# Kernel optimization log

Measured on AMD Instinct MI355X. Metric: run time of the kernel, lower is better.

Reference implementation:

```python
import jax, jax.numpy as jnp
import numpy as np

B, D, N_NEG, N_DOMAINS = 4096, 512, 100, 8
TAU = 1e-4
EPS = 1e-6
REG_W = 1e-4
ALPHA = 0.9


def setup_inputs() -> dict:
    key = jax.random.key(0)
    ks = jax.random.split(key, 12)
    e1 = jax.random.normal(ks[0], (B, D), dtype=jnp.float32)
    e2 = jax.random.normal(ks[1], (B, D), dtype=jnp.float32)
    y_pred = jax.random.normal(ks[2], (B, 1), dtype=jnp.float32)
    y_target = jax.random.normal(ks[3], (B, 1), dtype=jnp.float32)
    # e2_model: Linear(D, D); extra head params only contribute to the L2 reg term
    W_e2 = jax.random.normal(ks[4], (D, D), dtype=jnp.float32) * 0.02
    b_e2 = jax.random.normal(ks[5], (D,), dtype=jnp.float32) * 0.02
    W_head = jax.random.normal(ks[6], (D, 1), dtype=jnp.float32) * 0.02
    b_head = jax.random.normal(ks[7], (1,), dtype=jnp.float32) * 0.02
    # mixup coefficient lambda = (1-alpha)*U[0,1) + alpha, per sample
    lmbda = ALPHA + (1.0 - ALPHA) * jax.random.uniform(ks[8], (B,), dtype=jnp.float32)
    # mixup partner: random index != j (matches vec_neg exclusion in create_aug)
    off = jax.random.randint(ks[9], (B,), 1, B, dtype=jnp.int32)
    mix_idx = (jnp.arange(B, dtype=jnp.int32) + off) % B
    # n random negatives per sample for L_aug
    neg_idx = jax.random.randint(ks[10], (B, N_NEG), 0, B, dtype=jnp.int32)
    domain_tag = jax.random.randint(ks[11], (B,), 0, N_DOMAINS, dtype=jnp.int32)
    return {"e1": e1, "e2": e2, "y_pred": y_pred, "y_target": y_target,
            "W_e2": W_e2, "b_e2": b_e2, "W_head": W_head, "b_head": b_head,
            "lmbda": lmbda, "mix_idx": mix_idx, "neg_idx": neg_idx,
            "domain_tag": domain_tag}


def reference(e1, e2, y_pred, y_target, W_e2, b_e2, W_head, b_head,
              lmbda, mix_idx, neg_idx, domain_tag):
    # --- mse + L2 regularization over all model params ---
    mse_loss = jnp.mean((y_pred - y_target) ** 2)
    reg_loss = REG_W * (jnp.linalg.norm(W_e2) + jnp.linalg.norm(b_e2)
                        + jnp.linalg.norm(W_head) + jnp.linalg.norm(b_head))

    # --- create_aug: per-sample mixup, then phi_aug = e2_model(aug) ---
    aug = lmbda[:, None] * e1 + (1.0 - lmbda)[:, None] * e1[mix_idx]  # [B,D]
    phi_aug = aug @ W_e2 + b_e2                                       # [B,D]

    # --- L_aug: InfoNCE-style MI ratio, vectorized over the batch ---
    # S[j,k] = z_j . phi_A_k
    S = e2 @ phi_aug.T                                                # [B,B]
    pos = jnp.exp(TAU * jnp.diagonal(S))                              # [B]
    neg = jnp.exp(TAU * jnp.take_along_axis(S, neg_idx, axis=1))      # [B,n]
    L_a = jnp.log(pos / (EPS + pos + jnp.sum(neg, axis=1)))
    L_a = jnp.where(jnp.isnan(L_a), 0.0, L_a)  # original skips NaN terms
    aug_loss = -jnp.sum(L_a) / B

    # --- L_supp: cross-domain support ratio ---
    Ss = jnp.exp(TAU * (e2 @ e2.T))                                   # [B,B]
    diff_dom = domain_tag[:, None] != domain_tag[None, :]             # [B,B]
    nom = jnp.sum(jnp.where(diff_dom, Ss, 0.0), axis=1)
    den = jnp.sum(Ss, axis=1)
    L_s = jnp.log(nom / (den + EPS))
    valid = diff_dom.any(axis=1) & ~jnp.isnan(L_s)  # skip empty Z_D / NaN
    supp_loss = -jnp.sum(jnp.where(valid, L_s, 0.0)) / B

    # aug/supp use .item() in the original -> detached scalars
    return jnp.stack([mse_loss, reg_loss,
                      jax.lax.stop_gradient(aug_loss),
                      jax.lax.stop_gradient(supp_loss)])
```

## Files before the change

### kernel.cpp

```cpp
#include <hip/hip_runtime.h>
#include <hip/hip_bf16.h>
#include <math.h>

#define B_N 4096
#define D_N 512
#define N_NEGS 100
#define N_DOM 8
#define TAU_F 1e-4f
#define EPS_F 1e-6f
#define REGW_F 1e-4f
#define ITEMS_J 101
#define SEXP_LD 102

typedef __attribute__((ext_vector_type(8))) short bf16x8;
typedef __attribute__((ext_vector_type(4))) float f32x4;
typedef __attribute__((ext_vector_type(2))) float f32x2;

#define PHIF8_B 0u
#define E2B_B   (2u << 20)
#define WTB_B   (6u << 20)
#define AUGB_B  (WTB_B + (1u << 19))
#define SEXP_B  (AUGB_B + (4u << 20))
#define PDEN_B  (SEXP_B + (2u << 20))
#define PNOM_B  (PDEN_B + (1u << 19))
#define E2F8_B  (PNOM_B + (1u << 19))
#define STAT_B  (E2F8_B + (2u << 20))
#define S_MSE  0
#define S_B2   1
#define S_WH2  2
#define S_BH2  3
#define S_HIST 8
#define S_W2P  16
#define S_FIN  144

__device__ __forceinline__ ushort f2bf(float f) {
    union { __hip_bfloat16 h; ushort u; } v;
    v.h = __float2bfloat16(f);
    return v.u;
}
__device__ __forceinline__ float bf2f(short s) {
    return __uint_as_float(((uint)(ushort)s) << 16);
}

__device__ __forceinline__ void stage_bf16_tile(
        const ushort* __restrict__ g, int row0, int col0, int ldg,
        ushort* lds, int t) {
    int wid = t >> 6, lane = t & 63;
    #pragma unroll
    for (int i = 0; i < 4; ++i) {
        int p = i * 4096 + wid * 1024 + lane * 16;
        int row = p >> 7;
        int colb = (p & 127) ^ ((row & 7) << 4);
        const ushort* src = g + (size_t)(row0 + row) * ldg + col0 + (colb >> 1);
        ushort* dst = lds + (i * 4096 + wid * 1024) / 2;
        __builtin_amdgcn_global_load_lds(
            (const __attribute__((address_space(1))) unsigned int*)src,
            (__attribute__((address_space(3))) unsigned int*)dst, 16, 0, 0);
    }
}
__device__ __forceinline__ void stage_bf16_tile64(
        const ushort* __restrict__ g, int row0, int col0, int ldg,
        ushort* lds, int t) {
    int wid = t >> 6, lane = t & 63;
    #pragma unroll
    for (int i = 0; i < 2; ++i) {
        int p = i * 4096 + wid * 1024 + lane * 16;
        int row = p >> 7;
        int colb = (p & 127) ^ ((row & 7) << 4);
        const ushort* src = g + (size_t)(row0 + row) * ldg + col0 + (colb >> 1);
        ushort* dst = lds + (i * 4096 + wid * 1024) / 2;
        __builtin_amdgcn_global_load_lds(
            (const __attribute__((address_space(1))) unsigned int*)src,
            (__attribute__((address_space(3))) unsigned int*)dst, 16, 0, 0);
    }
}
__device__ __forceinline__ void stage_fp8_tile(
        const unsigned char* __restrict__ g, int row0, int col0, int ldg,
        unsigned char* lds, int t) {
    int wid = t >> 6, lane = t & 63;
    #pragma unroll
    for (int i = 0; i < 4; ++i) {
        int p = i * 4096 + wid * 1024 + lane * 16;
        int row = p >> 7;
        int colb = (p & 127) ^ ((row & 7) << 4);
        const unsigned char* src = g + (size_t)(row0 + row) * ldg + col0 + colb;
        unsigned char* dst = lds + i * 4096 + wid * 1024;
        __builtin_amdgcn_global_load_lds(
            (const __attribute__((address_space(1))) unsigned int*)src,
            (__attribute__((address_space(3))) unsigned int*)dst, 16, 0, 0);
    }
}

__device__ __forceinline__ float block_sum256(float v, float* sred) {
    #pragma unroll
    for (int m = 32; m; m >>= 1) v += __shfl_xor(v, m, 64);
    int lane = threadIdx.x & 63, wid = threadIdx.x >> 6;
    __syncthreads();
    if (lane == 0) sred[wid] = v;
    __syncthreads();
    float s = 0.0f;
    if (threadIdx.x == 0) s = sred[0] + sred[1] + sred[2] + sred[3];
    return s;
}

__global__ __launch_bounds__(256) void prep_kernel(
        const float* __restrict__ y_pred, const float* __restrict__ y_target,
        const float* __restrict__ W_e2, const float* __restrict__ b_e2,
        const float* __restrict__ W_head, const float* __restrict__ b_head,
        const float* __restrict__ e2, const float* __restrict__ e1,
        const float* __restrict__ lmbda, const int* __restrict__ mix,
        const int* __restrict__ tag,
        ushort* __restrict__ wtb, ushort* __restrict__ e2b,
        ushort* __restrict__ augb, unsigned char* __restrict__ e2f8,
        float* __restrict__ stat) {
    int t = threadIdx.x, x = blockIdx.x, job = blockIdx.y;
    if (job == 2) {
        int i = (x * 256 + t) * 8;
        f32x4 v0 = *(const f32x4*)(e2 + i);
        f32x4 v1 = *(const f32x4*)(e2 + i + 4);
        bf16x8 o;
        o[0] = (short)f2bf(v0.x); o[1] = (short)f2bf(v0.y);
        o[2] = (short)f2bf(v0.z); o[3] = (short)f2bf(v0.w);
        o[4] = (short)f2bf(v1.x); o[5] = (short)f2bf(v1.y);
        o[6] = (short)f2bf(v1.z); o[7] = (short)f2bf(v1.w);
        *(bf16x8*)(e2b + i) = o;
        return;
    }
    if (job == 4) {
        int i = (x * 256 + t) * 8;
        f32x4 v0 = *(const f32x4*)(e2 + i);
        f32x4 v1 = *(const f32x4*)(e2 + i + 4);
        int w0 = 0, w1 = 0;
        w0 = __builtin_amdgcn_cvt_pk_fp8_f32(v0.x, v0.y, w0, false);
        w0 = __builtin_amdgcn_cvt_pk_fp8_f32(v0.z, v0.w, w0, true);
        w1 = __builtin_amdgcn_cvt_pk_fp8_f32(v1.x, v1.y, w1, false);
        w1 = __builtin_amdgcn_cvt_pk_fp8_f32(v1.z, v1.w, w1, true);
        *(int2*)(e2f8 + i) = make_int2(w0, w1);
        return;
    }
    if (job == 3) {
        int i = (x * 256 + t) * 8;
        int row = i >> 9, col = i & 511;
        float lam = lmbda[row], oml = 1.0f - lam;
        const float* a = e1 + (size_t)row * D_N + col;
        const float* c = e1 + (size_t)mix[row] * D_N + col;
        f32x4 a0 = *(const f32x4*)a, a1 = *(const f32x4*)(a + 4);
        f32x4 c0 = *(const f32x4*)c, c1 = *(const f32x4*)(c + 4);
        bf16x8 o;
        o[0] = (short)f2bf(lam * a0.x + oml * c0.x);
        o[1] = (short)f2bf(lam * a0.y + oml * c0.y);
        o[2] = (short)f2bf(lam * a0.z + oml * c0.z);
        o[3] = (short)f2bf(lam * a0.w + oml * c0.w);
        o[4] = (short)f2bf(lam * a1.x + oml * c1.x);
        o[5] = (short)f2bf(lam * a1.y + oml * c1.y);
        o[6] = (short)f2bf(lam * a1.z + oml * c1.z);
        o[7] = (short)f2bf(lam * a1.w + oml * c1.w);
        *(bf16x8*)(augb + i) = o;
        return;
    }
    if (job == 1) {
        if (x >= 64) return;
        __shared__ float tile[64][65];
        int k0 = (x >> 3) * 64, n0 = (x & 7) * 64;
        int r = t >> 4, c = (t & 15) * 4;
        #pragma unroll
        for (int i = 0; i < 4; ++i) {
            f32x4 v = *(const f32x4*)(W_e2 + (size_t)(k0 + r + i * 16) * D_N + n0 + c);
            tile[r + i * 16][c]     = v.x;
            tile[r + i * 16][c + 1] = v.y;
            tile[r + i * 16][c + 2] = v.z;
            tile[r + i * 16][c + 3] = v.w;
        }
        __syncthreads();
        int nl = t >> 2, kq = (t & 3) * 16;
        bf16x8 o0, o1;
        #pragma unroll
        for (int q = 0; q < 8; ++q) o0[q] = (short)f2bf(tile[kq + q][nl]);
        #pragma unroll
        for (int q = 0; q < 8; ++q) o1[q] = (short)f2bf(tile[kq + 8 + q][nl]);
        ushort* dst = wtb + (size_t)(n0 + nl) * D_N + k0 + kq;
        *(bf16x8*)dst = o0;
        *(bf16x8*)(dst + 8) = o1;
        return;
    }
    __shared__ float sred[4];
    if (x < 128) {
        float s = 0.0f;
        for (int i = x * 256 + t; i < D_N * D_N; i += 128 * 256) {
            float w = W_e2[i]; s += w * w;
        }
        s = block_sum256(s, sred);
        if (t == 0) stat[S_W2P + x] = s;
    } else if (x == 128) {
        float s = 0.0f;
        for (int i = t; i < B_N; i += 256) {
            float d = y_pred[i] - y_target[i]; s += d * d;
        }
        s = block_sum256(s, sred);
        if (t == 0) stat[S_MSE] = s;
    } else if (x == 129) {
        float v1 = b_e2[t], v2 = b_e2[t + 256];
        float s = block_sum256(v1 * v1 + v2 * v2, sred);
        if (t == 0) stat[S_B2] = s;
        v1 = W_head[t]; v2 = W_head[t + 256];
        s = block_sum256(v1 * v1 + v2 * v2, sred);
        if (t == 0) {
            stat[S_WH2] = s;
            stat[S_BH2] = b_head[0] * b_head[0];
        }
    } else if (x == 130) {
        __shared__ int h[N_DOM];
        if (t < N_DOM) h[t] = 0;
        __syncthreads();
        for (int i = t; i < B_N; i += 256) atomicAdd(&h[tag[i]], 1);
        __syncthreads();
        if (t < N_DOM) stat[S_HIST + t] = (float)h[t];
    }
}

__global__ __launch_bounds__(256) void phi_kernel(
        const ushort* __restrict__ augb, const ushort* __restrict__ wtb,
        const float* __restrict__ bvec, unsigned char* __restrict__ phif8) {
    __shared__ ushort As[64 * 64];
    __shared__ ushort Bs[128 * 64];
    int rb = blockIdx.y * 64, cb = blockIdx.x * 128;
    int t = threadIdx.x;
    int lane = t & 63, wid = t >> 6;
    int l15 = lane & 15, g = lane >> 4, x7 = l15 & 7;
    int wr = wid >> 1, wc = wid & 1;

    f32x4 acc[2][4] = {};
    for (int kk = 0; kk < D_N; kk += 64) {
        __syncthreads();
        stage_bf16_tile64(augb, rb, kk, D_N, As, t);
        stage_bf16_tile  (wtb,  cb, kk, D_N, Bs, t);
        __syncthreads();
        bf16x8 a[2][2], b[4][2];
        #pragma unroll
        for (int mi = 0; mi < 2; ++mi)
            #pragma unroll
            for (int ks = 0; ks < 2; ++ks) {
                int ar = wr * 32 + mi * 16 + l15;
                a[mi][ks] = *(const bf16x8*)((const char*)As +
                    ar * 128 + (((ks << 2) | g) ^ x7) * 16);
            }
        #pragma unroll
        for (int ni = 0; ni < 4; ++ni)
            #pragma unroll
            for (int ks = 0; ks < 2; ++ks) {
                int br = wc * 64 + ni * 16 + l15;
                b[ni][ks] = *(const bf16x8*)((const char*)Bs +
                    br * 128 + (((ks << 2) | g) ^ x7) * 16);
            }
        #pragma unroll
        for (int mi = 0; mi < 2; ++mi)
            #pragma unroll
            for (int ni = 0; ni < 4; ++ni)
                #pragma unroll
                for (int ks = 0; ks < 2; ++ks)
                    acc[mi][ni] = __builtin_amdgcn_mfma_f32_16x16x32_bf16(
                        a[mi][ks], b[ni][ks], acc[mi][ni], 0, 0, 0);
    }
    float bb[4];
    #pragma unroll
    for (int ni = 0; ni < 4; ++ni) bb[ni] = bvec[cb + wc * 64 + ni * 16 + l15];
    #pragma unroll
    for (int mi = 0; mi < 2; ++mi)
        #pragma unroll
        for (int r = 0; r < 4; ++r) {
            int row = rb + wr * 32 + mi * 16 + g * 4 + r;
            #pragma unroll
            for (int ni = 0; ni < 4; ++ni) {
                int col = cb + wc * 64 + ni * 16 + l15;
                float v = acc[mi][ni][r] + bb[ni];
                phif8[(size_t)row * D_N + col] = (unsigned char)
                    (__builtin_amdgcn_cvt_pk_fp8_f32(v, v, 0, false) & 0xff);
            }
        }
}

__global__ __launch_bounds__(256) void supp_kernel(
        const unsigned char* __restrict__ e2f8, const int* __restrict__ tag,
        float* __restrict__ pden, float* __restrict__ pnom) {
    __shared__ unsigned char As8[128 * 128];
    __shared__ unsigned char Bs8[128 * 128];
    __shared__ int rt_s[128], ct_s[128];

    int tid = blockIdx.x;
    int sw = (tid & 7) * 66 + (tid >> 3);
    int by = (int)((sqrtf(8.0f * (float)sw + 1.0f) - 1.0f) * 0.5f);
    while ((by + 1) * (by + 2) / 2 <= sw) ++by;
    while (by * (by + 1) / 2 > sw) --by;
    int bx = sw - by * (by + 1) / 2;
    bool diag = (bx == by);
    int rb = by * 128, cb = bx * 128;
    int t = threadIdx.x;
    if (t < 128) rt_s[t] = tag[rb + t];
    else         ct_s[t - 128] = tag[cb + t - 128];

    int lane = t & 63, wid = t >> 6;
    int l15 = lane & 15, g = lane >> 4, x7 = l15 & 7;
    int wr = wid >> 1, wc = wid & 1;

    f32x4 acc[4][4] = {};
    for (int kk = 0; kk < D_N; kk += 128) {
        __syncthreads();
        stage_fp8_tile(e2f8, rb, kk, D_N, As8, t);
        stage_fp8_tile(e2f8, cb, kk, D_N, Bs8, t);
        __syncthreads();
        long a[4][4], b[4][4];
        #pragma unroll
        for (int mi = 0; mi < 4; ++mi) {
            int ar = wr * 64 + mi * 16 + l15;
            int br = wc * 64 + mi * 16 + l15;
            #pragma unroll
            for (int ks = 0; ks < 4; ++ks) {
                int off = (ks * 32 + g * 8) ^ (x7 << 4);
                a[mi][ks] = *(const long*)(As8 + ar * 128 + off);
                b[mi][ks] = *(const long*)(Bs8 + br * 128 + off);
            }
        }
        #pragma unroll
        for (int mi = 0; mi < 4; ++mi)
            #pragma unroll
            for (int ni = 0; ni < 4; ++ni)
                #pragma unroll
                for (int ks = 0; ks < 4; ++ks)
                    acc[mi][ni] = __builtin_amdgcn_mfma_f32_16x16x32_fp8_fp8(
                        a[mi][ks], b[ni][ks], acc[mi][ni], 0, 0, 0);
    }
    int ct[4];
    #pragma unroll
    for (int ni = 0; ni < 4; ++ni) ct[ni] = ct_s[wc * 64 + ni * 16 + l15];
    float cd[4] = {}, cn[4] = {};
    #pragma unroll
    for (int mi = 0; mi < 4; ++mi) {
        #pragma unroll
        for (int r = 0; r < 4; ++r) {
            int row = wr * 64 + mi * 16 + g * 4 + r;
            int rt = rt_s[row];
            float d = 0.f, n = 0.f;
            #pragma unroll
            for (int ni = 0; ni < 4; ++ni) {
                float v = __expf(TAU_F * acc[mi][ni][r]);
                float nv = (ct[ni] != rt) ? v : 0.f;
                d += v; n += nv;
                cd[ni] += v; cn[ni] += nv;
            }
            #pragma unroll
            for (int mm = 1; mm < 16; mm <<= 1) {
                d += __shfl_xor(d, mm);
                n += __shfl_xor(n, mm);
            }
            if (l15 == 0) {
                pden[bx * B_N + rb + row] = d;
                pnom[bx * B_N + rb + row] = n;
            }
        }
    }
    if (!diag) {
        #pragma unroll
        for (int ni = 0; ni < 4; ++ni) {
            float d = cd[ni], n = cn[ni];
            d += __shfl_xor(d, 16); d += __shfl_xor(d, 32);
            n += __shfl_xor(n, 16); n += __shfl_xor(n, 32);
            if (g == 0) {
                int col = wc * 64 + ni * 16 + l15;
                pden[by * B_N + cb + col] = d;
                pnom[by * B_N + cb + col] = n;
            }
        }
    }
}

__global__ __launch_bounds__(256, 4) void aug_dots_kernel(
        const ushort* __restrict__ e2b, const unsigned char* __restrict__ phif8,
        const int* __restrict__ neg_idx, float* __restrict__ sexp) {
    int gi = blockIdx.x * 32 + (threadIdx.x >> 3);
    int sub = threadIdx.x & 7;
    int j = gi / ITEMS_J;
    int idx = gi - j * ITEMS_J;
    int tgt = (idx == 0) ? j : neg_idx[(size_t)j * N_NEGS + idx - 1];
    const ushort* e        = e2b   + (size_t)j   * D_N + sub * 8;
    const unsigned char* p = phif8 + (size_t)tgt * D_N + sub * 8;

    uint2 pv[8]; bf16x8 ev[8];
    #pragma unroll
    for (int k = 0; k < 8; ++k) {
        pv[k] = *(const uint2*)(p + k * 64);
        ev[k] = *(const bf16x8*)(e + k * 64);
    }
    float s0 = 0.f, s1 = 0.f;
    #pragma unroll
    for (int k = 0; k < 8; ++k) {
        f32x2 a0 = __builtin_amdgcn_cvt_pk_f32_fp8((int)pv[k].x, false);
        f32x2 a1 = __builtin_amdgcn_cvt_pk_f32_fp8((int)pv[k].x, true);
        f32x2 a2 = __builtin_amdgcn_cvt_pk_f32_fp8((int)pv[k].y, false);
        f32x2 a3 = __builtin_amdgcn_cvt_pk_f32_fp8((int)pv[k].y, true);
        s0 += bf2f(ev[k][0]) * a0.x + bf2f(ev[k][1]) * a0.y
            + bf2f(ev[k][2]) * a1.x + bf2f(ev[k][3]) * a1.y;
        s1 += bf2f(ev[k][4]) * a2.x + bf2f(ev[k][5]) * a2.y
            + bf2f(ev[k][6]) * a3.x + bf2f(ev[k][7]) * a3.y;
    }
    float s = s0 + s1;
    s += __shfl_xor(s, 1);
    s += __shfl_xor(s, 2);
    s += __shfl_xor(s, 4);
    if (sub == 0) sexp[(size_t)j * SEXP_LD + idx] = __expf(TAU_F * s);
}

__global__ __launch_bounds__(256) void final1_kernel(
        const float* __restrict__ sexp, const float* __restrict__ pden,
        const float* __restrict__ pnom, const int* __restrict__ tag,
        float* __restrict__ stat) {
    __shared__ float wla[4], wls[4];
    int lane = threadIdx.x & 63, w = threadIdx.x >> 6;
    int j0 = blockIdx.x * 64;
    float la = 0.f, ls = 0.f;
    for (int jj = w; jj < 64; jj += 4) {
        int j = j0 + jj;
        float v0 = sexp[(size_t)j * SEXP_LD + lane];
        float v1 = (lane + 64 < ITEMS_J) ? sexp[(size_t)j * SEXP_LD + lane + 64] : 0.f;
        float pos = __shfl(v0, 0);
        float ns = ((lane >= 1) ? v0 : 0.f) + v1;
        float d = (lane < 32) ? pden[lane * B_N + j] : 0.f;
        float n = (lane < 32) ? pnom[lane * B_N + j] : 0.f;
        #pragma unroll
        for (int mm = 32; mm; mm >>= 1) {
            ns += __shfl_xor(ns, mm);
            d  += __shfl_xor(d, mm);
            n  += __shfl_xor(n, mm);
        }
        if (lane == 0) {
            float La = logf(pos / (EPS_F + pos + ns));
            if (La == La) la += La;
            float Ls = logf(n / (d + EPS_F));
            bool valid = (stat[S_HIST + tag[j]] < (float)B_N) && (Ls == Ls);
            if (valid) ls += Ls;
        }
    }
    if (lane == 0) { wla[w] = la; wls[w] = ls; }
    __syncthreads();
    if (threadIdx.x == 0) {
        stat[S_FIN + blockIdx.x * 2]     = wla[0] + wla[1] + wla[2] + wla[3];
        stat[S_FIN + blockIdx.x * 2 + 1] = wls[0] + wls[1] + wls[2] + wls[3];
    }
}

__global__ __launch_bounds__(256) void final2_kernel(
        const float* __restrict__ stat, float* __restrict__ out) {
    __shared__ float sred[4];
    int t = threadIdx.x;
    float w2 = block_sum256(t < 128 ? stat[S_W2P + t] : 0.f, sred);
    float la = block_sum256(t < 64 ? stat[S_FIN + 2 * t] : 0.f, sred);
    float ls = block_sum256(t < 64 ? stat[S_FIN + 2 * t + 1] : 0.f, sred);
    if (t == 0) {
        out[0] = stat[S_MSE] / (float)B_N;
        out[1] = REGW_F * (sqrtf(w2) + sqrtf(stat[S_B2]) +
                           sqrtf(stat[S_WH2]) + sqrtf(stat[S_BH2]));
        out[2] = -la / (float)B_N;
        out[3] = -ls / (float)B_N;
    }
}

extern "C" void kernel_launch(void* const* d_in, const int* in_sizes, int n_in,
                              void* d_out, int out_size, void* d_ws, size_t ws_size,
                              hipStream_t stream) {
    const float* e1       = (const float*)d_in[0];
    const float* e2       = (const float*)d_in[1];
    const float* y_pred   = (const float*)d_in[2];
    const float* y_target = (const float*)d_in[3];
    const float* W_e2     = (const float*)d_in[4];
    const float* b_e2     = (const float*)d_in[5];
    const float* W_head   = (const float*)d_in[6];
    const float* b_head   = (const float*)d_in[7];
    const float* lmbda    = (const float*)d_in[8];
    const int*   mix_idx  = (const int*)d_in[9];
    const int*   neg_idx  = (const int*)d_in[10];
    const int*   dtag     = (const int*)d_in[11];
    char* base = (char*)d_ws;
    float* out = (float*)d_out;
    unsigned char* phif8 = (unsigned char*)(base + PHIF8_B);
    ushort* e2b  = (ushort*)(base + E2B_B);
    ushort* wtb  = (ushort*)(base + WTB_B);
    ushort* augb = (ushort*)(base + AUGB_B);
    float*  sexp = (float*)(base + SEXP_B);
    float*  pden = (float*)(base + PDEN_B);
    float*  pnom = (float*)(base + PNOM_B);
    unsigned char* e2f8 = (unsigned char*)(base + E2F8_B);
    float*  stat = (float*)(base + STAT_B);

    prep_kernel<<<dim3(1024, 5), dim3(256), 0, stream>>>(
        y_pred, y_target, W_e2, b_e2, W_head, b_head, e2, e1, lmbda, mix_idx,
        dtag, wtb, e2b, augb, e2f8, stat);
    phi_kernel<<<dim3(D_N / 128, B_N / 64), dim3(256), 0, stream>>>(
        augb, wtb, b_e2, phif8);
    supp_kernel<<<dim3(528), dim3(256), 0, stream>>>(e2f8, dtag, pden, pnom);
    aug_dots_kernel<<<dim3(B_N * ITEMS_J / 32), dim3(256), 0, stream>>>(
        e2b, phif8, neg_idx, sexp);
    final1_kernel<<<dim3(64), dim3(256), 0, stream>>>(
        sexp, pden, pnom, dtag, stat);
    final2_kernel<<<dim3(1), dim3(256), 0, stream>>>(stat, out);
}
```

Before: 87.97 us.

## Merge phi and supp GEMMs into one launch and compact prep grid

The independent phi (mixup projection) GEMM and the e2·e2ᵀ support GEMM now run as one kernel, with block ranges picking the task. Both run concurrently and one launch is saved. The prep kernel's 2D grid, which had many idle blocks, becomes a compact 1D grid. The bf16 and fp8 e2 conversions are merged so e2 is read once, and the W_e2 squared-norm is folded into the transpose blocks instead of a separate pass. The cost is a larger shared-memory footprint for the phi blocks, which may lower their occupancy.

```diff
diff --git a/kernel.cpp b/kernel.cpp
--- a/kernel.cpp
+++ b/kernel.cpp
@@ -11,6 +11,7 @@
 #define REGW_F 1e-4f
 #define ITEMS_J 101
 #define SEXP_LD 102
+#define SUPP_NB 528
 
 typedef __attribute__((ext_vector_type(8))) short bf16x8;
 typedef __attribute__((ext_vector_type(4))) float f32x4;
@@ -113,8 +114,8 @@
         ushort* __restrict__ wtb, ushort* __restrict__ e2b,
         ushort* __restrict__ augb, unsigned char* __restrict__ e2f8,
         float* __restrict__ stat) {
-    int t = threadIdx.x, x = blockIdx.x, job = blockIdx.y;
-    if (job == 2) {
+    int t = threadIdx.x, x = blockIdx.x;
+    if (x < 1024) {
         int i = (x * 256 + t) * 8;
         f32x4 v0 = *(const f32x4*)(e2 + i);
         f32x4 v1 = *(const f32x4*)(e2 + i + 4);
@@ -124,12 +125,6 @@
         o[4] = (short)f2bf(v1.x); o[5] = (short)f2bf(v1.y);
         o[6] = (short)f2bf(v1.z); o[7] = (short)f2bf(v1.w);
         *(bf16x8*)(e2b + i) = o;
-        return;
-    }
-    if (job == 4) {
-        int i = (x * 256 + t) * 8;
-        f32x4 v0 = *(const f32x4*)(e2 + i);
-        f32x4 v1 = *(const f32x4*)(e2 + i + 4);
         int w0 = 0, w1 = 0;
         w0 = __builtin_amdgcn_cvt_pk_fp8_f32(v0.x, v0.y, w0, false);
         w0 = __builtin_amdgcn_cvt_pk_fp8_f32(v0.z, v0.w, w0, true);
@@ -138,8 +133,8 @@
         *(int2*)(e2f8 + i) = make_int2(w0, w1);
         return;
     }
-    if (job == 3) {
-        int i = (x * 256 + t) * 8;
+    if (x < 2048) {
+        int i = ((x - 1024) * 256 + t) * 8;
         int row = i >> 9, col = i & 511;
         float lam = lmbda[row], oml = 1.0f - lam;
         const float* a = e1 + (size_t)row * D_N + col;
@@ -158,11 +153,13 @@
         *(bf16x8*)(augb + i) = o;
         return;
     }
-    if (job == 1) {
-        if (x >= 64) return;
+    if (x < 2112) {
+        int xx = x - 2048;
         __shared__ float tile[64][65];
-        int k0 = (x >> 3) * 64, n0 = (x & 7) * 64;
+        __shared__ float sred[4];
+        int k0 = (xx >> 3) * 64, n0 = (xx & 7) * 64;
         int r = t >> 4, c = (t & 15) * 4;
+        float ss = 0.0f;
         #pragma unroll
         for (int i = 0; i < 4; ++i) {
             f32x4 v = *(const f32x4*)(W_e2 + (size_t)(k0 + r + i * 16) * D_N + n0 + c);
@@ -170,6 +167,7 @@
             tile[r + i * 16][c + 1] = v.y;
             tile[r + i * 16][c + 2] = v.z;
             tile[r + i * 16][c + 3] = v.w;
+            ss += v.x * v.x + v.y * v.y + v.z * v.z + v.w * v.w;
         }
         __syncthreads();
         int nl = t >> 2, kq = (t & 3) * 16;
@@ -181,24 +179,19 @@
         ushort* dst = wtb + (size_t)(n0 + nl) * D_N + k0 + kq;
         *(bf16x8*)dst = o0;
         *(bf16x8*)(dst + 8) = o1;
+        float s = block_sum256(ss, sred);
+        if (t == 0) stat[S_W2P + xx] = s;
         return;
     }
     __shared__ float sred[4];
-    if (x < 128) {
-        float s = 0.0f;
-        for (int i = x * 256 + t; i < D_N * D_N; i += 128 * 256) {
-            float w = W_e2[i]; s += w * w;
-        }
-        s = block_sum256(s, sred);
-        if (t == 0) stat[S_W2P + x] = s;
-    } else if (x == 128) {
+    if (x == 2112) {
         float s = 0.0f;
         for (int i = t; i < B_N; i += 256) {
             float d = y_pred[i] - y_target[i]; s += d * d;
         }
         s = block_sum256(s, sred);
         if (t == 0) stat[S_MSE] = s;
-    } else if (x == 129) {
+    } else if (x == 2113) {
         float v1 = b_e2[t], v2 = b_e2[t + 256];
         float s = block_sum256(v1 * v1 + v2 * v2, sred);
         if (t == 0) stat[S_B2] = s;
@@ -208,7 +201,7 @@
             stat[S_WH2] = s;
             stat[S_BH2] = b_head[0] * b_head[0];
         }
-    } else if (x == 130) {
+    } else if (x == 2114) {
         __shared__ int h[N_DOM];
         if (t < N_DOM) h[t] = 0;
         __syncthreads();
@@ -218,73 +211,75 @@
     }
 }
 
-__global__ __launch_bounds__(256) void phi_kernel(
+__global__ __launch_bounds__(256) void gemm_kernel(
+        const unsigned char* __restrict__ e2f8, const int* __restrict__ tag,
         const ushort* __restrict__ augb, const ushort* __restrict__ wtb,
-        const float* __restrict__ bvec, unsigned char* __restrict__ phif8) {
-    __shared__ ushort As[64 * 64];
-    __shared__ ushort Bs[128 * 64];
-    int rb = blockIdx.y * 64, cb = blockIdx.x * 128;
+        const float* __restrict__ bvec,
+        float* __restrict__ pden, float* __restrict__ pnom,
+        unsigned char* __restrict__ phif8) {
+    __shared__ unsigned char As8[128 * 128];
+    __shared__ unsigned char Bs8[128 * 128];
+    __shared__ int rt_s[128], ct_s[128];
     int t = threadIdx.x;
     int lane = t & 63, wid = t >> 6;
     int l15 = lane & 15, g = lane >> 4, x7 = l15 & 7;
     int wr = wid >> 1, wc = wid & 1;
 
-    f32x4 acc[2][4] = {};
-    for (int kk = 0; kk < D_N; kk += 64) {
-        __syncthreads();
-        stage_bf16_tile64(augb, rb, kk, D_N, As, t);
-        stage_bf16_tile  (wtb,  cb, kk, D_N, Bs, t);
-        __syncthreads();
-        bf16x8 a[2][2], b[4][2];
-        #pragma unroll
-        for (int mi = 0; mi < 2; ++mi)
-            #pragma unroll
-            for (int ks = 0; ks < 2; ++ks) {
-                int ar = wr * 32 + mi * 16 + l15;
-                a[mi][ks] = *(const bf16x8*)((const char*)As +
-                    ar * 128 + (((ks << 2) | g) ^ x7) * 16);
-            }
-        #pragma unroll
-        for (int ni = 0; ni < 4; ++ni)
-            #pragma unroll
-            for (int ks = 0; ks < 2; ++ks) {
-                int br = wc * 64 + ni * 16 + l15;
-                b[ni][ks] = *(const bf16x8*)((const char*)Bs +
-                    br * 128 + (((ks << 2) | g) ^ x7) * 16);
-            }
-        #pragma unroll
-        for (int mi = 0; mi < 2; ++mi)
+    if (blockIdx.x >= SUPP_NB) {
+        int bid = blockIdx.x - SUPP_NB;
+        int rb = (bid >> 2) * 64, cb = (bid & 3) * 128;
+        ushort* As = (ushort*)As8;
+        ushort* Bs = (ushort*)Bs8;
+        f32x4 acc[2][4] = {};
+        for (int kk = 0; kk < D_N; kk += 64) {
+            __syncthreads();
+            stage_bf16_tile64(augb, rb, kk, D_N, As, t);
+            stage_bf16_tile  (wtb,  cb, kk, D_N, Bs, t);
+            __syncthreads();
+            bf16x8 a[2][2], b[4][2];
+            #pragma unroll
+            for (int mi = 0; mi < 2; ++mi)
+                #pragma unroll
+                for (int ks = 0; ks < 2; ++ks) {
+                    int ar = wr * 32 + mi * 16 + l15;
+                    a[mi][ks] = *(const bf16x8*)((const char*)As +
+                        ar * 128 + (((ks << 2) | g) ^ x7) * 16);
+                }
             #pragma unroll
             for (int ni = 0; ni < 4; ++ni)
                 #pragma unroll
-                for (int ks = 0; ks < 2; ++ks)
-                    acc[mi][ni] = __builtin_amdgcn_mfma_f32_16x16x32_bf16(
-                        a[mi][ks], b[ni][ks], acc[mi][ni], 0, 0, 0);
-    }
-    float bb[4];
-    #pragma unroll
-    for (int ni = 0; ni < 4; ++ni) bb[ni] = bvec[cb + wc * 64 + ni * 16 + l15];
-    #pragma unroll
-    for (int mi = 0; mi < 2; ++mi)
-        #pragma unroll
-        for (int r = 0; r < 4; ++r) {
-            int row = rb + wr * 32 + mi * 16 + g * 4 + r;
-            #pragma unroll
-            for (int ni = 0; ni < 4; ++ni) {
-                int col = cb + wc * 64 + ni * 16 + l15;
-                float v = acc[mi][ni][r] + bb[ni];
-                phif8[(size_t)row * D_N + col] = (unsigned char)
-                    (__builtin_amdgcn_cvt_pk_fp8_f32(v, v, 0, false) & 0xff);
-            }
-        }
-}
-
-__global__ __launch_bounds__(256) void supp_kernel(
-        const unsigned char* __restrict__ e2f8, const int* __restrict__ tag,
-        float* __restrict__ pden, float* __restrict__ pnom) {
-    __shared__ unsigned char As8[128 * 128];
-    __shared__ unsigned char Bs8[128 * 128];
-    __shared__ int rt_s[128], ct_s[128];
+                for (int ks = 0; ks < 2; ++ks) {
+                    int br = wc * 64 + ni * 16 + l15;
+                    b[ni][ks] = *(const bf16x8*)((const char*)Bs +
+                        br * 128 + (((ks << 2) | g) ^ x7) * 16);
+                }
+            #pragma unroll
+            for (int mi = 0; mi < 2; ++mi)
+                #pragma unroll
+                for (int ni = 0; ni < 4; ++ni)
+                    #pragma unroll
+                    for (int ks = 0; ks < 2; ++ks)
+                        acc[mi][ni] = __builtin_amdgcn_mfma_f32_16x16x32_bf16(
+                            a[mi][ks], b[ni][ks], acc[mi][ni], 0, 0, 0);
+        }
+        float bb[4];
+        #pragma unroll
+        for (int ni = 0; ni < 4; ++ni) bb[ni] = bvec[cb + wc * 64 + ni * 16 + l15];
+        #pragma unroll
+        for (int mi = 0; mi < 2; ++mi)
+            #pragma unroll
+            for (int r = 0; r < 4; ++r) {
+                int row = rb + wr * 32 + mi * 16 + g * 4 + r;
+                #pragma unroll
+                for (int ni = 0; ni < 4; ++ni) {
+                    int col = cb + wc * 64 + ni * 16 + l15;
+                    float v = acc[mi][ni][r] + bb[ni];
+                    phif8[(size_t)row * D_N + col] = (unsigned char)
+                        (__builtin_amdgcn_cvt_pk_fp8_f32(v, v, 0, false) & 0xff);
+                }
+            }
+        return;
+    }
 
     int tid = blockIdx.x;
     int sw = (tid & 7) * 66 + (tid >> 3);
@@ -294,13 +289,8 @@
     int bx = sw - by * (by + 1) / 2;
     bool diag = (bx == by);
     int rb = by * 128, cb = bx * 128;
-    int t = threadIdx.x;
     if (t < 128) rt_s[t] = tag[rb + t];
     else         ct_s[t - 128] = tag[cb + t - 128];
-
-    int lane = t & 63, wid = t >> 6;
-    int l15 = lane & 15, g = lane >> 4, x7 = l15 & 7;
-    int wr = wid >> 1, wc = wid & 1;
 
     f32x4 acc[4][4] = {};
     for (int kk = 0; kk < D_N; kk += 128) {
@@ -451,7 +441,7 @@
         const float* __restrict__ stat, float* __restrict__ out) {
     __shared__ float sred[4];
     int t = threadIdx.x;
-    float w2 = block_sum256(t < 128 ? stat[S_W2P + t] : 0.f, sred);
+    float w2 = block_sum256(t < 64 ? stat[S_W2P + t] : 0.f, sred);
     float la = block_sum256(t < 64 ? stat[S_FIN + 2 * t] : 0.f, sred);
     float ls = block_sum256(t < 64 ? stat[S_FIN + 2 * t + 1] : 0.f, sred);
     if (t == 0) {
@@ -490,12 +480,11 @@
     unsigned char* e2f8 = (unsigned char*)(base + E2F8_B);
     float*  stat = (float*)(base + STAT_B);
 
-    prep_kernel<<<dim3(1024, 5), dim3(256), 0, stream>>>(
+    prep_kernel<<<dim3(2115), dim3(256), 0, stream>>>(
         y_pred, y_target, W_e2, b_e2, W_head, b_head, e2, e1, lmbda, mix_idx,
         dtag, wtb, e2b, augb, e2f8, stat);
-    phi_kernel<<<dim3(D_N / 128, B_N / 64), dim3(256), 0, stream>>>(
-        augb, wtb, b_e2, phif8);
-    supp_kernel<<<dim3(528), dim3(256), 0, stream>>>(e2f8, dtag, pden, pnom);
+    gemm_kernel<<<dim3(SUPP_NB + 256), dim3(256), 0, stream>>>(
+        e2f8, dtag, augb, wtb, b_e2, pden, pnom, phif8);
     aug_dots_kernel<<<dim3(B_N * ITEMS_J / 32), dim3(256), 0, stream>>>(
         e2b, phif8, neg_idx, sexp);
     final1_kernel<<<dim3(64), dim3(256), 0, stream>>>(
```

Result: faster. 81.15 us (-7.8%).
